# Optimization experiments

Measured on AMD Instinct MI355X. Metric: run time of the kernel, lower is better.

The kernel has to match this reference:

```python
import jax, jax.numpy as jnp
import numpy as np

B, F_DIM, C, M = 16, 64, 64, 512
OUT_CH = 32
DT = 1.0


def setup_inputs() -> dict:
    key = jax.random.key(0)
    ks = jax.random.split(key, 8)
    x = jax.random.normal(ks[0], (B, F_DIM, C, M), dtype=jnp.float32)
    A = jax.random.uniform(ks[1], (B, M, C, C), dtype=jnp.float32)
    phys_prior = jax.random.normal(ks[2], (B, C, M), dtype=jnp.float32)
    kappa = jnp.array(0.1, dtype=jnp.float32)
    alpha = jnp.array(0.05, dtype=jnp.float32)
    # r_phi MLP: Linear(1,16) -> ELU -> Linear(16,1)
    w1 = jax.random.normal(ks[3], (16, 1), dtype=jnp.float32) * 1.0
    b1 = jnp.zeros((16,), dtype=jnp.float32)
    w2 = jax.random.normal(ks[4], (1, 16), dtype=jnp.float32) * 0.25
    b2 = jnp.zeros((1,), dtype=jnp.float32)
    # 1x1 Conv2d(1, OUT_CH): weight (OUT_CH,1,1,1) -> flatten to (OUT_CH,)
    pw = jax.random.normal(ks[5], (OUT_CH,), dtype=jnp.float32)
    pb = jnp.zeros((OUT_CH,), dtype=jnp.float32)
    return {"x": x, "A": A, "phys_prior": phys_prior, "kappa": kappa,
            "alpha": alpha, "w1": w1, "b1": b1, "w2": w2, "b2": b2,
            "pw": pw, "pb": pb}


def reference(x, A, phys_prior, kappa, alpha, w1, b1, w2, b2, pw, pb):
    # x: (B,F,C,M), A: (B,M,C,C), phys_prior: (B,C,M)
    s = x.mean(axis=1)                      # (B,C,M)
    deg = A.sum(axis=-1)                    # (B,M,C)
    sT = jnp.transpose(s, (0, 2, 1))        # (B,M,C)
    # torch einsum 'bmcd,bmcn->bmdn' with n=1 contracts over c: (A^T s)
    As = jnp.einsum('bmcd,bmc->bmd', A, sT)  # (B,M,C)
    Ls = jnp.transpose(deg * sT - As, (0, 2, 1))  # (B,C,M)
    k = jax.nn.softplus(kappa)
    # tiny MLP on per-(b,c) mean over M
    r_in = s.mean(axis=-1, keepdims=True)   # (B,C,1)
    h = jax.nn.elu(r_in @ w1.T + b1)        # (B,C,16)
    r = h @ w2.T + b2                       # (B,C,1), broadcasts over M
    phys_corr = alpha * phys_prior          # (B,C,M)
    s_new = s - DT * k * Ls + DT * (r + phys_corr)  # (B,C,M)
    # 1x1 conv over (B,1,C,M): pointwise scale+bias per output channel
    corr = s_new[:, None, :, :] * pw[None, :, None, None] + pb[None, :, None, None]
    return corr  # (B,OUT_CH,C,M)
```

## Files before the change

### kernel.cpp

```cpp
#include <hip/hip_runtime.h>
#include <math.h>

#define B_  16
#define F_  64
#define C_  64
#define M_  512
#define OC_ 32

typedef float vf4 __attribute__((ext_vector_type(4)));

__global__ __launch_bounds__(128, 6) void k1_mean(
    const float* __restrict__ x,
    float* __restrict__ s_out, float* __restrict__ rpart)
{
    const int gid = blockIdx.x;
    const int q   = gid & 3;
    const int bc  = gid >> 2;
    const int b   = bc >> 6;
    const int c   = bc & 63;
    const int t   = threadIdx.x;
    const int tf  = t >> 5;
    const int tm  = t & 31;
    const int m4  = (q << 5) + tm;

    const size_t rowbase = ((size_t)b * F_ * C_ + c) * M_;
    float ax = 0.f, ay = 0.f, az = 0.f, aw = 0.f;
    #pragma unroll 8
    for (int j = 0; j < 16; ++j) {
        const int f = (tf << 4) + j;
        const float4 v = ((const float4*)(x + rowbase + (size_t)f * C_ * M_))[m4];
        ax += v.x; ay += v.y; az += v.z; aw += v.w;
    }

    __shared__ float4 red[4][32];
    red[tf][tm] = make_float4(ax, ay, az, aw);
    __syncthreads();

    if (tf == 0) {
        const float4 r1 = red[1][tm], r2 = red[2][tm], r3 = red[3][tm];
        const float inv_f = 1.0f / (float)F_;
        float4 sv;
        sv.x = (ax + r1.x + r2.x + r3.x) * inv_f;
        sv.y = (ay + r1.y + r2.y + r3.y) * inv_f;
        sv.z = (az + r1.z + r2.z + r3.z) * inv_f;
        sv.w = (aw + r1.w + r2.w + r3.w) * inv_f;
        ((float4*)(s_out + (size_t)bc * M_))[m4] = sv;

        float p = sv.x + sv.y + sv.z + sv.w;
        #pragma unroll
        for (int off = 16; off > 0; off >>= 1) p += __shfl_xor(p, off);
        if (t == 0) rpart[gid] = p;
    }
}

__global__ __launch_bounds__(256) void k2_laplace(
    const float* __restrict__ A, const float* __restrict__ phys,
    const float* __restrict__ kappa_p, const float* __restrict__ alpha_p,
    const float* __restrict__ s_in, const float* __restrict__ rpart,
    const float* __restrict__ w1, const float* __restrict__ b1,
    const float* __restrict__ w2, const float* __restrict__ b2,
    float* __restrict__ snew)
{
    __shared__ float Al[C_ * 65];
    __shared__ float sl[C_];
    __shared__ float redD[4 * C_];
    __shared__ float redA[4 * C_];

    const int bm = blockIdx.x;
    const int b  = bm >> 9;
    const int m  = bm & 511;
    const int t  = threadIdx.x;
    const int c  = t & 63;
    const int q  = t >> 6;

    float r = 0.f;
    if (t < 64) {
        const float4 rp = ((const float4*)rpart)[b * C_ + t];
        const float rin = (rp.x + rp.y + rp.z + rp.w) * (1.0f / (float)M_);
        r = b2[0];
        #pragma unroll
        for (int j = 0; j < 16; ++j) {
            float h = rin * w1[j] + b1[j];
            h = (h > 0.f) ? h : (expf(h) - 1.f);
            r += h * w2[j];
        }
        sl[t] = s_in[((size_t)b * C_ + t) * M_ + m];
    }

    const float4* Ap = (const float4*)(A + (size_t)bm * (C_ * C_));
    #pragma unroll
    for (int i = 0; i < 4; ++i) {
        const int idx = t + i * 256;
        const float4 v = Ap[idx];
        const int row = idx >> 4;
        const int col = (idx & 15) << 2;
        float* dst = &Al[row * 65 + col];
        dst[0] = v.x; dst[1] = v.y; dst[2] = v.z; dst[3] = v.w;
    }
    __syncthreads();

    float dpart = 0.f, apart = 0.f;
    const int j0 = q << 4;
    #pragma unroll
    for (int j = 0; j < 16; ++j) {
        dpart += Al[c * 65 + (j0 + j)];
        apart += Al[(j0 + j) * 65 + c] * sl[j0 + j];
    }
    redD[(q << 6) + c] = dpart;
    redA[(q << 6) + c] = apart;
    __syncthreads();

    if (t < 64) {
        const float deg = redD[t] + redD[64 + t] + redD[128 + t] + redD[192 + t];
        const float As  = redA[t] + redA[64 + t] + redA[128 + t] + redA[192 + t];
        const float sval = sl[t];
        const float k    = log1pf(expf(kappa_p[0]));
        const float Ls   = deg * sval - As;
        const float val  = sval - k * Ls
                         + (r + alpha_p[0] * phys[((size_t)b * C_ + t) * M_ + m]);
        snew[((size_t)b * C_ + t) * M_ + m] = val;
    }
}

__global__ __launch_bounds__(256) void k3_expand(
    const float* __restrict__ snew,
    const float* __restrict__ pw, const float* __restrict__ pb,
    float* __restrict__ out)
{
    const int n4 = (B_ * OC_ * C_ * M_) / 4;
    for (int i = blockIdx.x * blockDim.x + threadIdx.x; i < n4;
         i += gridDim.x * blockDim.x) {
        const int m4 = i & 127;
        const int c  = (i >> 7) & 63;
        const int o  = (i >> 13) & 31;
        const int b  = i >> 18;
        const float4 v = ((const float4*)snew)[(((b << 6) + c) << 7) + m4];
        const float w  = pw[o];
        const float bb = pb[o];
        vf4 r;
        r.x = v.x * w + bb; r.y = v.y * w + bb;
        r.z = v.z * w + bb; r.w = v.w * w + bb;
        __builtin_nontemporal_store(r, ((vf4*)out) + i);
    }
}

extern "C" void kernel_launch(void* const* d_in, const int* in_sizes, int n_in,
                              void* d_out, int out_size, void* d_ws, size_t ws_size,
                              hipStream_t stream)
{
    const float* x     = (const float*)d_in[0];
    const float* A     = (const float*)d_in[1];
    const float* phys  = (const float*)d_in[2];
    const float* kappa = (const float*)d_in[3];
    const float* alpha = (const float*)d_in[4];
    const float* w1    = (const float*)d_in[5];
    const float* b1    = (const float*)d_in[6];
    const float* w2    = (const float*)d_in[7];
    const float* b2    = (const float*)d_in[8];
    const float* pw    = (const float*)d_in[9];
    const float* pb    = (const float*)d_in[10];
    float* out = (float*)d_out;

    float* ws    = (float*)d_ws;
    float* s     = ws;
    float* snew  = ws + (size_t)B_ * C_ * M_;
    float* rpart = ws + (size_t)2 * B_ * C_ * M_;

    k1_mean<<<B_ * C_ * 4, 128, 0, stream>>>(x, s, rpart);
    k2_laplace<<<B_ * M_, 256, 0, stream>>>(A, phys, kappa, alpha, s, rpart,
                                            w1, b1, w2, b2, snew);
    k3_expand<<<2048, 256, 0, stream>>>(snew, pw, pb, out);
}
```

Baseline: 65.71 us.

## Store snew transposed in k2 and transpose through LDS in k3

k2 now writes s_new in (b,m,c) order, so its 64 threads make one contiguous store per block instead of stride-M scattered stores. k3 becomes a tiled kernel: each block loads a 16x64 snewT tile into padded shared memory, transposes it, and writes all 32 output channels from registers. This removes the uncoalesced writes in k2 and reuses each loaded value across the channels. The cost is fewer blocks in k3 (512) and an extra LDS round trip with a barrier.

```diff
diff --git a/kernel.cpp b/kernel.cpp
--- a/kernel.cpp
+++ b/kernel.cpp
@@ -59,7 +59,7 @@
     const float* __restrict__ s_in, const float* __restrict__ rpart,
     const float* __restrict__ w1, const float* __restrict__ b1,
     const float* __restrict__ w2, const float* __restrict__ b2,
-    float* __restrict__ snew)
+    float* __restrict__ snewT)
 {
     __shared__ float Al[C_ * 65];
     __shared__ float sl[C_];
@@ -118,29 +118,47 @@
         const float Ls   = deg * sval - As;
         const float val  = sval - k * Ls
                          + (r + alpha_p[0] * phys[((size_t)b * C_ + t) * M_ + m]);
-        snew[((size_t)b * C_ + t) * M_ + m] = val;
+        snewT[((size_t)bm) * C_ + t] = val;
     }
 }
 
 __global__ __launch_bounds__(256) void k3_expand(
-    const float* __restrict__ snew,
+    const float* __restrict__ snewT,
     const float* __restrict__ pw, const float* __restrict__ pb,
     float* __restrict__ out)
 {
-    const int n4 = (B_ * OC_ * C_ * M_) / 4;
-    for (int i = blockIdx.x * blockDim.x + threadIdx.x; i < n4;
-         i += gridDim.x * blockDim.x) {
-        const int m4 = i & 127;
-        const int c  = (i >> 7) & 63;
-        const int o  = (i >> 13) & 31;
-        const int b  = i >> 18;
-        const float4 v = ((const float4*)snew)[(((b << 6) + c) << 7) + m4];
+    __shared__ float sn[16 * 65];
+
+    const int blk = blockIdx.x;
+    const int b   = blk >> 5;
+    const int m0  = (blk & 31) << 4;
+    const int t   = threadIdx.x;
+
+    {
+        const float4 v = ((const float4*)(snewT + ((size_t)(b * M_ + m0)) * C_))[t];
+        const int row = t >> 4;
+        const int col = (t & 15) << 2;
+        float* dst = &sn[row * 65 + col];
+        dst[0] = v.x; dst[1] = v.y; dst[2] = v.z; dst[3] = v.w;
+    }
+    __syncthreads();
+
+    const int c   = t >> 2;
+    const int m4r = t & 3;
+    const float v0 = sn[(4 * m4r + 0) * 65 + c];
+    const float v1 = sn[(4 * m4r + 1) * 65 + c];
+    const float v2 = sn[(4 * m4r + 2) * 65 + c];
+    const float v3 = sn[(4 * m4r + 3) * 65 + c];
+
+    const size_t obase = ((size_t)b * OC_ * C_ + c) * M_ + m0 + (m4r << 2);
+    #pragma unroll 8
+    for (int o = 0; o < OC_; ++o) {
         const float w  = pw[o];
         const float bb = pb[o];
         vf4 r;
-        r.x = v.x * w + bb; r.y = v.y * w + bb;
-        r.z = v.z * w + bb; r.w = v.w * w + bb;
-        __builtin_nontemporal_store(r, ((vf4*)out) + i);
+        r.x = v0 * w + bb; r.y = v1 * w + bb;
+        r.z = v2 * w + bb; r.w = v3 * w + bb;
+        __builtin_nontemporal_store(r, (vf4*)(out + obase + (size_t)o * (C_ * M_)));
     }
 }
 
@@ -163,11 +181,11 @@
 
     float* ws    = (float*)d_ws;
     float* s     = ws;
-    float* snew  = ws + (size_t)B_ * C_ * M_;
+    float* snewT = ws + (size_t)B_ * C_ * M_;
     float* rpart = ws + (size_t)2 * B_ * C_ * M_;
 
     k1_mean<<<B_ * C_ * 4, 128, 0, stream>>>(x, s, rpart);
     k2_laplace<<<B_ * M_, 256, 0, stream>>>(A, phys, kappa, alpha, s, rpart,
-                                            w1, b1, w2, b2, snew);
-    k3_expand<<<2048, 256, 0, stream>>>(snew, pw, pb, out);
+                                            w1, b1, w2, b2, snewT);
+    k3_expand<<<B_ * (M_ / 16), 256, 0, stream>>>(snewT, pw, pb, out);
 }
```

After: 67.54 us. 2.8% more time.

## Double-buffer A tiles via async global-to-LDS loads, four m per block

Applied to the files above, without the earlier changes.

The Laplacian kernel now processes four consecutive m values per block. It stages each 64x64 A tile straight into LDS with global_load_lds, prefetching the next tile while computing on the current one. Row degrees are computed with a shuffle-based transpose-reduction instead of strided LDS reads, and phys and snew are accessed as float4. The aim is to overlap A streaming with compute and to cut per-block overhead. The cost is more complex synchronisation, and it relies on the barrier covering completion of the asynchronous LDS writes.

```diff
diff --git a/kernel.cpp b/kernel.cpp
--- a/kernel.cpp
+++ b/kernel.cpp
@@ -53,7 +53,19 @@
     }
 }
 
-__global__ __launch_bounds__(256) void k2_laplace(
+__device__ __forceinline__ void stage_tile(const float* g, float* l, int w, int lane)
+{
+    #pragma unroll
+    for (int i = 0; i < 4; ++i) {
+        const float* gp = g + (((w << 2) + i) << 8) + (lane << 2);
+        float*       lp = l + (((w << 2) + i) << 8);
+        __builtin_amdgcn_global_load_lds(
+            (const __attribute__((address_space(1))) void*)gp,
+            (__attribute__((address_space(3))) void*)lp, 16, 0, 0);
+    }
+}
+
+__global__ __launch_bounds__(256, 4) void k2_async(
     const float* __restrict__ A, const float* __restrict__ phys,
     const float* __restrict__ kappa_p, const float* __restrict__ alpha_p,
     const float* __restrict__ s_in, const float* __restrict__ rpart,
@@ -61,64 +73,117 @@
     const float* __restrict__ w2, const float* __restrict__ b2,
     float* __restrict__ snew)
 {
-    __shared__ float Al[C_ * 65];
-    __shared__ float sl[C_];
-    __shared__ float redD[4 * C_];
-    __shared__ float redA[4 * C_];
-
-    const int bm = blockIdx.x;
-    const int b  = bm >> 9;
-    const int m  = bm & 511;
-    const int t  = threadIdx.x;
-    const int c  = t & 63;
-    const int q  = t >> 6;
-
-    float r = 0.f;
+    __shared__ float Abuf[2][4096];
+    __shared__ float sl[4 * C_];
+    __shared__ float redA[2][4 * C_];
+    __shared__ float degL[2][C_];
+
+    const int t   = threadIdx.x;
+    const int c   = t & 63;
+    const int q   = t >> 6;
+    const int blk = blockIdx.x;
+    const int b   = blk >> 7;
+    const int m0  = (blk & 127) << 2;
+    const int j0  = q << 4;
+
+    const float* Ab = A + (size_t)(b * M_ + m0) * (C_ * C_);
+
+    stage_tile(Ab, &Abuf[0][0], q, c);
+
+    sl[t] = s_in[((size_t)(b * C_ + c)) * M_ + m0 + q];
+    const float kcoef = log1pf(expf(kappa_p[0]));
+    const float al    = alpha_p[0];
+    float r_c = 0.f;
+    float4 ph4 = make_float4(0.f, 0.f, 0.f, 0.f);
     if (t < 64) {
         const float4 rp = ((const float4*)rpart)[b * C_ + t];
         const float rin = (rp.x + rp.y + rp.z + rp.w) * (1.0f / (float)M_);
-        r = b2[0];
+        r_c = b2[0];
         #pragma unroll
         for (int j = 0; j < 16; ++j) {
-            float h = rin * w1[j] + b1[j];
-            h = (h > 0.f) ? h : (expf(h) - 1.f);
-            r += h * w2[j];
-        }
-        sl[t] = s_in[((size_t)b * C_ + t) * M_ + m];
-    }
-
-    const float4* Ap = (const float4*)(A + (size_t)bm * (C_ * C_));
+            float hh = rin * w1[j] + b1[j];
+            hh = (hh > 0.f) ? hh : (expf(hh) - 1.f);
+            r_c += hh * w2[j];
+        }
+        ph4 = *(const float4*)(phys + ((size_t)(b * C_ + t)) * M_ + m0);
+    }
+    __syncthreads();
+
+    float out_v[4];
     #pragma unroll
-    for (int i = 0; i < 4; ++i) {
-        const int idx = t + i * 256;
-        const float4 v = Ap[idx];
-        const int row = idx >> 4;
-        const int col = (idx & 15) << 2;
-        float* dst = &Al[row * 65 + col];
-        dst[0] = v.x; dst[1] = v.y; dst[2] = v.z; dst[3] = v.w;
-    }
-    __syncthreads();
-
-    float dpart = 0.f, apart = 0.f;
-    const int j0 = q << 4;
-    #pragma unroll
-    for (int j = 0; j < 16; ++j) {
-        dpart += Al[c * 65 + (j0 + j)];
-        apart += Al[(j0 + j) * 65 + c] * sl[j0 + j];
-    }
-    redD[(q << 6) + c] = dpart;
-    redA[(q << 6) + c] = apart;
-    __syncthreads();
+    for (int mi = 0; mi < 4; ++mi) {
+        const int cur = mi & 1;
+        if (mi < 3) stage_tile(Ab + (size_t)(mi + 1) * (C_ * C_),
+                               &Abuf[cur ^ 1][0], q, c);
+
+        float sv[16];
+        #pragma unroll
+        for (int kq = 0; kq < 4; ++kq) {
+            const float4 s4 = *(const float4*)&sl[mi * 64 + j0 + (kq << 2)];
+            sv[kq * 4 + 0] = s4.x; sv[kq * 4 + 1] = s4.y;
+            sv[kq * 4 + 2] = s4.z; sv[kq * 4 + 3] = s4.w;
+        }
+
+        float v[16];
+        float ap = 0.f;
+        #pragma unroll
+        for (int k = 0; k < 16; ++k) {
+            const float a = Abuf[cur][(j0 + k) * 64 + c];
+            ap += a * sv[k];
+            v[k] = a;
+        }
+
+        #pragma unroll
+        for (int k = 0; k < 16; ++k) v[k] += __shfl_xor(v[k], 32);
+        #pragma unroll
+        for (int k = 0; k < 16; ++k) v[k] += __shfl_xor(v[k], 16);
+        const int h = c & 15;
+        float e[8];
+        #pragma unroll
+        for (int kk = 0; kk < 8; ++kk) {
+            const float sd = (h & 8) ? v[kk] : v[kk + 8];
+            const float rv = __shfl_xor(sd, 8);
+            e[kk] = ((h & 8) ? v[kk + 8] : v[kk]) + rv;
+        }
+        float f2[4];
+        #pragma unroll
+        for (int kk = 0; kk < 4; ++kk) {
+            const float sd = (h & 4) ? e[kk] : e[kk + 4];
+            const float rv = __shfl_xor(sd, 4);
+            f2[kk] = ((h & 4) ? e[kk + 4] : e[kk]) + rv;
+        }
+        float g2[2];
+        #pragma unroll
+        for (int kk = 0; kk < 2; ++kk) {
+            const float sd = (h & 2) ? f2[kk] : f2[kk + 2];
+            const float rv = __shfl_xor(sd, 2);
+            g2[kk] = ((h & 2) ? f2[kk + 2] : f2[kk]) + rv;
+        }
+        float D;
+        {
+            const float sd = (h & 1) ? g2[0] : g2[1];
+            const float rv = __shfl_xor(sd, 1);
+            D = ((h & 1) ? g2[1] : g2[0]) + rv;
+        }
+
+        redA[cur][(q << 6) + c] = ap;
+        if (c < 16) degL[cur][j0 + c] = D;
+        __syncthreads();
+
+        if (t < 64) {
+            const float As = redA[cur][t] + redA[cur][64 + t]
+                           + redA[cur][128 + t] + redA[cur][192 + t];
+            const float dg = degL[cur][t];
+            const float sval = sl[mi * 64 + t];
+            const float pv = (mi == 0) ? ph4.x : (mi == 1) ? ph4.y
+                           : (mi == 2) ? ph4.z : ph4.w;
+            out_v[mi] = sval - kcoef * (dg * sval - As) + (r_c + al * pv);
+        }
+    }
 
     if (t < 64) {
-        const float deg = redD[t] + redD[64 + t] + redD[128 + t] + redD[192 + t];
-        const float As  = redA[t] + redA[64 + t] + redA[128 + t] + redA[192 + t];
-        const float sval = sl[t];
-        const float k    = log1pf(expf(kappa_p[0]));
-        const float Ls   = deg * sval - As;
-        const float val  = sval - k * Ls
-                         + (r + alpha_p[0] * phys[((size_t)b * C_ + t) * M_ + m]);
-        snew[((size_t)b * C_ + t) * M_ + m] = val;
+        *(float4*)(snew + ((size_t)(b * C_ + t)) * M_ + m0) =
+            make_float4(out_v[0], out_v[1], out_v[2], out_v[3]);
     }
 }
 
@@ -167,7 +232,7 @@
     float* rpart = ws + (size_t)2 * B_ * C_ * M_;
 
     k1_mean<<<B_ * C_ * 4, 128, 0, stream>>>(x, s, rpart);
-    k2_laplace<<<B_ * M_, 256, 0, stream>>>(A, phys, kappa, alpha, s, rpart,
-                                            w1, b1, w2, b2, snew);
+    k2_async<<<B_ * (M_ / 4), 256, 0, stream>>>(A, phys, kappa, alpha, s, rpart,
+                                                w1, b1, w2, b2, snew);
     k3_expand<<<2048, 256, 0, stream>>>(snew, pw, pb, out);
 }
```

Result: slower. 69.90 us (+6.4%).

## Fuse Laplacian update with output expansion and pipeline A tiles per block

Applied to the files above, without the earlier changes.

Merges the Laplacian/update kernel and the 1x1-conv expansion kernel into one. Each 1024-thread block processes 16 consecutive m positions and double-buffers A matrices through shared memory with register prefetch. The intermediate s_new stays in shared memory instead of round-tripping through global memory, and one launch is removed. In exchange, the grid is much smaller, each matrix step needs two block-wide barriers, and output stores become 64-byte row segments rather than fully contiguous streams.

```diff
diff --git a/kernel.cpp b/kernel.cpp
--- a/kernel.cpp
+++ b/kernel.cpp
@@ -53,94 +53,117 @@
     }
 }
 
-__global__ __launch_bounds__(256) void k2_laplace(
+__global__ __launch_bounds__(1024, 8) void k2_fused(
     const float* __restrict__ A, const float* __restrict__ phys,
     const float* __restrict__ kappa_p, const float* __restrict__ alpha_p,
     const float* __restrict__ s_in, const float* __restrict__ rpart,
     const float* __restrict__ w1, const float* __restrict__ b1,
     const float* __restrict__ w2, const float* __restrict__ b2,
-    float* __restrict__ snew)
+    const float* __restrict__ pw, const float* __restrict__ pb,
+    float* __restrict__ out)
 {
-    __shared__ float Al[C_ * 65];
-    __shared__ float sl[C_];
-    __shared__ float redD[4 * C_];
-    __shared__ float redA[4 * C_];
+    __shared__ float Ab[2][4096];
+    __shared__ float sl[16 * 68];
+    __shared__ float ph[16 * 68];
+    __shared__ float snl[64 * 17];
+    __shared__ float redA[16 * 64];
+    __shared__ float degL[C_];
 
-    const int bm = blockIdx.x;
-    const int b  = bm >> 9;
-    const int m  = bm & 511;
-    const int t  = threadIdx.x;
-    const int c  = t & 63;
-    const int q  = t >> 6;
+    const int t   = threadIdx.x;
+    const int blk = blockIdx.x;
+    const int b   = blk >> 5;
+    const int m0  = (blk & 31) << 4;
 
-    float r = 0.f;
+    {
+        const int cc = t >> 4;
+        const int mi = t & 15;
+        const size_t g = ((size_t)(b * C_ + cc)) * M_ + m0 + mi;
+        sl[mi * 68 + cc] = s_in[g];
+        ph[mi * 68 + cc] = phys[g];
+    }
+
+    float r_c = 0.f;
     if (t < 64) {
         const float4 rp = ((const float4*)rpart)[b * C_ + t];
         const float rin = (rp.x + rp.y + rp.z + rp.w) * (1.0f / (float)M_);
-        r = b2[0];
+        r_c = b2[0];
         #pragma unroll
         for (int j = 0; j < 16; ++j) {
-            float h = rin * w1[j] + b1[j];
-            h = (h > 0.f) ? h : (expf(h) - 1.f);
-            r += h * w2[j];
+            float hh = rin * w1[j] + b1[j];
+            hh = (hh > 0.f) ? hh : (expf(hh) - 1.f);
+            r_c += hh * w2[j];
         }
-        sl[t] = s_in[((size_t)b * C_ + t) * M_ + m];
     }
 
-    const float4* Ap = (const float4*)(A + (size_t)bm * (C_ * C_));
-    #pragma unroll
-    for (int i = 0; i < 4; ++i) {
-        const int idx = t + i * 256;
-        const float4 v = Ap[idx];
-        const int row = idx >> 4;
-        const int col = (idx & 15) << 2;
-        float* dst = &Al[row * 65 + col];
-        dst[0] = v.x; dst[1] = v.y; dst[2] = v.z; dst[3] = v.w;
-    }
+    const float* Abase = A + (size_t)(b * M_ + m0) * (C_ * C_);
+    float4 v = ((const float4*)Abase)[t];
+    ((float4*)Ab[0])[t] = v;
     __syncthreads();
 
-    float dpart = 0.f, apart = 0.f;
-    const int j0 = q << 4;
+    const float kcoef = log1pf(expf(kappa_p[0]));
+    const float al    = alpha_p[0];
+    const int c   = t & 63;
+    const int g   = t >> 6;
+    const int row = t >> 4;
+    const int h   = t & 15;
+
+    #pragma unroll 1
+    for (int i = 0; i < 16; ++i) {
+        const int cur = i & 1;
+
+        float4 vn;
+        if (i < 15)
+            vn = ((const float4*)(Abase + (size_t)(i + 1) * (C_ * C_)))[t];
+
+        float p = v.x + v.y + v.z + v.w;
+        p += __shfl_xor(p, 1);
+        p += __shfl_xor(p, 2);
+        p += __shfl_xor(p, 4);
+        p += __shfl_xor(p, 8);
+        if (h == 0) degL[row] = p;
+
+        const float s0 = sl[i * 68 + 4 * g + 0];
+        const float s1 = sl[i * 68 + 4 * g + 1];
+        const float s2 = sl[i * 68 + 4 * g + 2];
+        const float s3 = sl[i * 68 + 4 * g + 3];
+        const float ap = Ab[cur][(4 * g + 0) * 64 + c] * s0
+                       + Ab[cur][(4 * g + 1) * 64 + c] * s1
+                       + Ab[cur][(4 * g + 2) * 64 + c] * s2
+                       + Ab[cur][(4 * g + 3) * 64 + c] * s3;
+        redA[g * 64 + c] = ap;
+        __syncthreads();
+
+        if (t < 64) {
+            float As = 0.f;
+            #pragma unroll
+            for (int gg = 0; gg < 16; ++gg) As += redA[gg * 64 + t];
+            const float dg   = degL[t];
+            const float sval = sl[i * 68 + t];
+            const float pv   = ph[i * 68 + t];
+            snl[t * 17 + i] = sval - kcoef * (dg * sval - As) + (r_c + al * pv);
+        }
+        if (i < 15) {
+            ((float4*)Ab[cur ^ 1])[t] = vn;
+            v = vn;
+        }
+        __syncthreads();
+    }
+
     #pragma unroll
-    for (int j = 0; j < 16; ++j) {
-        dpart += Al[c * 65 + (j0 + j)];
-        apart += Al[(j0 + j) * 65 + c] * sl[j0 + j];
-    }
-    redD[(q << 6) + c] = dpart;
-    redA[(q << 6) + c] = apart;
-    __syncthreads();
-
-    if (t < 64) {
-        const float deg = redD[t] + redD[64 + t] + redD[128 + t] + redD[192 + t];
-        const float As  = redA[t] + redA[64 + t] + redA[128 + t] + redA[192 + t];
-        const float sval = sl[t];
-        const float k    = log1pf(expf(kappa_p[0]));
-        const float Ls   = deg * sval - As;
-        const float val  = sval - k * Ls
-                         + (r + alpha_p[0] * phys[((size_t)b * C_ + t) * M_ + m]);
-        snew[((size_t)b * C_ + t) * M_ + m] = val;
-    }
-}
-
-__global__ __launch_bounds__(256) void k3_expand(
-    const float* __restrict__ snew,
-    const float* __restrict__ pw, const float* __restrict__ pb,
-    float* __restrict__ out)
-{
-    const int n4 = (B_ * OC_ * C_ * M_) / 4;
-    for (int i = blockIdx.x * blockDim.x + threadIdx.x; i < n4;
-         i += gridDim.x * blockDim.x) {
-        const int m4 = i & 127;
-        const int c  = (i >> 7) & 63;
-        const int o  = (i >> 13) & 31;
-        const int b  = i >> 18;
-        const float4 v = ((const float4*)snew)[(((b << 6) + c) << 7) + m4];
+    for (int i = 0; i < 8; ++i) {
+        const int idx = (i << 10) + t;
+        const int mq  = idx & 3;
+        const int cc  = (idx >> 2) & 63;
+        const int o   = idx >> 8;
         const float w  = pw[o];
         const float bb = pb[o];
-        vf4 r;
-        r.x = v.x * w + bb; r.y = v.y * w + bb;
-        r.z = v.z * w + bb; r.w = v.w * w + bb;
-        __builtin_nontemporal_store(r, ((vf4*)out) + i);
+        vf4 ov;
+        ov.x = snl[cc * 17 + mq * 4 + 0] * w + bb;
+        ov.y = snl[cc * 17 + mq * 4 + 1] * w + bb;
+        ov.z = snl[cc * 17 + mq * 4 + 2] * w + bb;
+        ov.w = snl[cc * 17 + mq * 4 + 3] * w + bb;
+        __builtin_nontemporal_store(ov,
+            (vf4*)(out + (((size_t)(b * OC_ + o)) * C_ + cc) * M_ + m0 + mq * 4));
     }
 }
 
@@ -163,11 +186,9 @@
 
     float* ws    = (float*)d_ws;
     float* s     = ws;
-    float* snew  = ws + (size_t)B_ * C_ * M_;
-    float* rpart = ws + (size_t)2 * B_ * C_ * M_;
+    float* rpart = ws + (size_t)B_ * C_ * M_;
 
     k1_mean<<<B_ * C_ * 4, 128, 0, stream>>>(x, s, rpart);
-    k2_laplace<<<B_ * M_, 256, 0, stream>>>(A, phys, kappa, alpha, s, rpart,
-                                            w1, b1, w2, b2, snew);
-    k3_expand<<<2048, 256, 0, stream>>>(snew, pw, pb, out);
+    k2_fused<<<B_ * (M_ / 16), 1024, 0, stream>>>(A, phys, kappa, alpha, s, rpart,
+                                                  w1, b1, w2, b2, pw, pb, out);
 }
```

Measured after the change: 65.37 us (median of 2 runs). Within noise of the previous version (-0.5%).
